# Kernel optimization log

Hardware: AMD Instinct MI355X
Metric: run time of the kernel (lower is better)

The kernel has to match this reference:

```python
import jax, jax.numpy as jnp
import numpy as np

PH = PW = 16  # patch size


def setup_inputs() -> dict:
    key = jax.random.key(0)
    k1, k2, k3, k4, k5 = jax.random.split(key, 5)
    B, N, D, V = 8, 4096, 768, 10240
    x = jax.random.uniform(k1, (B, N, D), dtype=jnp.float32)          # (B, N, ph*pw*C) in [0,1)
    patch_coord = jax.random.randint(k2, (B, N, 2), 0, 64).astype(jnp.int64)  # (y, x) grid coords
    patch_valid = jax.random.randint(k3, (B, N), 0, 2).astype(bool)
    proj_w = jax.random.normal(k4, (D, D), dtype=jnp.float32) * 0.02  # Linear weight (out, in), no bias
    pos_table = jax.random.normal(k5, (2, V, D), dtype=jnp.float32) * 0.02
    return {"x": x, "patch_coord": patch_coord, "patch_valid": patch_valid,
            "proj_w": proj_w, "pos_table": pos_table}


def reference(x, patch_coord, patch_valid, proj_w, pos_table):
    B, N, PPC = x.shape
    C = PPC // (PH * PW)
    # Reorder patch pixels from (ph, pw, C) flat order to (C, ph, pw) flat order.
    x = x.reshape(B, N, PH, PW, C).transpose(0, 1, 4, 2, 3).reshape(B, N, PPC)
    x = 2.0 * (x - 0.5)
    x = jnp.einsum('bnk,dk->bnd', x, proj_w)  # Linear, bias=False
    # External (y, x) -> internal (x, y)
    position_ids = patch_coord[..., ::-1]
    clamped = jnp.maximum(position_ids, 0)
    # Equivalent to one_hot(clamped) @ table summed over the 2 coord axes.
    pos = pos_table[0][clamped[..., 0]] + pos_table[1][clamped[..., 1]]  # (B, N, D)
    padding_positions = ~patch_valid
    pos = jnp.where(padding_positions[..., None], 0.0, pos)
    return x + pos, position_ids, padding_positions
```

## Files before the change

### kernel.cpp

```cpp
#include <hip/hip_runtime.h>
#include <hip/hip_bf16.h>
#include <cstddef>

#define D_DIM 768
#define V_DIM 10240
#define ROWS 32768
#define BM 128
#define BN 128
#define BK 32

using bf16x8 = __attribute__((ext_vector_type(8))) __bf16;
using f32x4  = __attribute__((ext_vector_type(4))) float;

__global__ void prep_w(const float* __restrict__ W, __bf16* __restrict__ Wp,
                       float* __restrict__ bias) {
    __shared__ float row[D_DIM];
    __shared__ float red[256];
    const int d = blockIdx.x;
    const int t = threadIdx.x;
    float s = 0.f;
    for (int k = t; k < D_DIM; k += 256) {
        float w = W[(size_t)d * D_DIM + k];
        row[k] = w;
        s += w;
    }
    red[t] = s;
    __syncthreads();
    for (int off = 128; off > 0; off >>= 1) {
        if (t < off) red[t] += red[t + off];
        __syncthreads();
    }
    if (t == 0) bias[d] = -red[0];
    for (int j = t; j < D_DIM; j += 256) {
        int c  = j % 3;
        int pw = (j / 3) & 15;
        int ph = j / 48;
        Wp[(size_t)d * D_DIM + j] = (__bf16)(2.0f * row[c * 256 + ph * 16 + pw]);
    }
}

__global__ void conv_aux(const float* __restrict__ X, __bf16* __restrict__ Xb,
                         const int* __restrict__ coord, const int* __restrict__ valid,
                         float* __restrict__ out1, float* __restrict__ out2) {
    int i = blockIdx.x * blockDim.x + threadIdx.x;
    size_t base = (size_t)i * 8;
    const float4* src = (const float4*)(X + base);
    float4 f0 = src[0];
    float4 f1 = src[1];
    bf16x8 v;
    v[0] = (__bf16)f0.x; v[1] = (__bf16)f0.y; v[2] = (__bf16)f0.z; v[3] = (__bf16)f0.w;
    v[4] = (__bf16)f1.x; v[5] = (__bf16)f1.y; v[6] = (__bf16)f1.z; v[7] = (__bf16)f1.w;
    *(bf16x8*)(Xb + base) = v;

    if (i < ROWS) {
        int c0 = coord[2 * i];
        int c1 = coord[2 * i + 1];
        out1[2 * i]     = (float)c1;
        out1[2 * i + 1] = (float)c0;
        out2[i] = valid[i] ? 0.0f : 1.0f;
    }
}

__global__ void aux_out(const int* __restrict__ coord, const int* __restrict__ valid,
                        float* __restrict__ out1, float* __restrict__ out2) {
    int i = blockIdx.x * blockDim.x + threadIdx.x;
    if (i < ROWS) {
        int c0 = coord[2 * i];
        int c1 = coord[2 * i + 1];
        out1[2 * i]     = (float)c1;
        out1[2 * i + 1] = (float)c0;
        out2[i] = valid[i] ? 0.0f : 1.0f;
    }
}

__launch_bounds__(256)
__global__ void gemm_fast(const __bf16* __restrict__ Xb, const __bf16* __restrict__ Wp,
                          const float* __restrict__ bias, const float* __restrict__ ptab,
                          const int* __restrict__ coord, const int* __restrict__ valid,
                          float* __restrict__ out) {
    __shared__ __align__(16) __bf16 la[BM * BK];
    __shared__ __align__(16) __bf16 lb[BN * BK];

    const int id  = blockIdx.x;
    const int xcd = id & 7;
    const int j6  = id >> 3;
    const int p   = xcd * 32 + j6 / 6;
    const int c   = j6 % 6;
    const int m0  = p * BM;
    const int n0  = c * BN;

    const int tid  = threadIdx.x;
    const int lane = tid & 63;
    const int wave = tid >> 6;
    const int wr   = (wave >> 1) * 64;
    const int wc   = (wave & 1) * 64;
    const int lr   = lane & 15;
    const int qh   = lane >> 4;

    const __bf16* srcA[2];
    const __bf16* srcB[2];
    int dst[2];
    #pragma unroll
    for (int i = 0; i < 2; ++i) {
        int q   = i * 256 + tid;
        int row = q >> 2;
        int un  = (q & 3) ^ ((row >> 1) & 3);
        srcA[i] = Xb + (size_t)(m0 + row) * D_DIM + un * 8;
        srcB[i] = Wp + (size_t)(n0 + row) * D_DIM + un * 8;
        dst[i]  = q * 8;
    }

    int aoff[4], boff[4];
    #pragma unroll
    for (int i = 0; i < 4; ++i) {
        int rowa = wr + i * 16 + lr;
        aoff[i] = rowa * BK + ((qh ^ ((rowa >> 1) & 3)) * 8);
        int rowb = wc + i * 16 + lr;
        boff[i] = rowb * BK + ((qh ^ ((rowb >> 1) & 3)) * 8);
    }

    f32x4 acc[4][4] = {};

    for (int kt = 0; kt < D_DIM / BK; ++kt) {
        const int k0 = kt * BK;

        #pragma unroll
        for (int i = 0; i < 2; ++i) {
            __builtin_amdgcn_global_load_lds(
                (const __attribute__((address_space(1))) void*)(srcA[i] + k0),
                (__attribute__((address_space(3))) void*)&la[dst[i]], 16, 0, 0);
            __builtin_amdgcn_global_load_lds(
                (const __attribute__((address_space(1))) void*)(srcB[i] + k0),
                (__attribute__((address_space(3))) void*)&lb[dst[i]], 16, 0, 0);
        }

        __syncthreads();

        bf16x8 af[4], bfr[4];
        #pragma unroll
        for (int i = 0; i < 4; ++i)
            af[i] = *(const bf16x8*)&la[aoff[i]];
        #pragma unroll
        for (int j = 0; j < 4; ++j)
            bfr[j] = *(const bf16x8*)&lb[boff[j]];

        #pragma unroll
        for (int i = 0; i < 4; ++i)
            #pragma unroll
            for (int j = 0; j < 4; ++j)
                acc[i][j] = __builtin_amdgcn_mfma_f32_16x16x32_bf16(af[i], bfr[j], acc[i][j], 0, 0, 0);

        __syncthreads();
    }

    const float* pt0 = ptab;
    const float* pt1 = ptab + (size_t)V_DIM * D_DIM;
    const int rq = (lane >> 4) * 4;

    float bvals[4];
    #pragma unroll
    for (int j = 0; j < 4; ++j)
        bvals[j] = bias[n0 + wc + j * 16 + lr];

    #pragma unroll
    for (int i = 0; i < 4; ++i) {
        #pragma unroll
        for (int r = 0; r < 4; ++r) {
            int m = m0 + wr + i * 16 + rq + r;
            int c0 = coord[2 * m];
            int c1 = coord[2 * m + 1];
            if (c0 < 0) c0 = 0;
            if (c1 < 0) c1 = 0;
            int vld = valid[m];
            #pragma unroll
            for (int j = 0; j < 4; ++j) {
                int d = n0 + wc + j * 16 + lr;
                float v = acc[i][j][r] + bvals[j];
                if (vld)
                    v += pt0[(size_t)c1 * D_DIM + d] + pt1[(size_t)c0 * D_DIM + d];
                out[(size_t)m * D_DIM + d] = v;
            }
        }
    }
}

__launch_bounds__(256)
__global__ void gemm_slow(const float* __restrict__ X, const __bf16* __restrict__ Wp,
                          const float* __restrict__ bias, const float* __restrict__ ptab,
                          const int* __restrict__ coord, const int* __restrict__ valid,
                          float* __restrict__ out) {
    __shared__ __align__(16) __bf16 la[BM * BK];
    __shared__ __align__(16) __bf16 lb[BN * BK];

    const int n0 = blockIdx.x * BN;
    const int m0 = blockIdx.y * BM;

    const int tid  = threadIdx.x;
    const int lane = tid & 63;
    const int wave = tid >> 6;
    const int wr   = (wave >> 1) * 64;
    const int wc   = (wave & 1) * 64;
    const int lr   = lane & 15;
    const int kq   = (lane >> 4) * 8;

    f32x4 acc[4][4] = {};

    for (int kt = 0; kt < D_DIM / BK; ++kt) {
        const int k0 = kt * BK;

        #pragma unroll
        for (int i = 0; i < 2; ++i) {
            int idx = i * 2048 + tid * 8;
            int row = idx >> 5;
            int col = idx & 31;
            const __bf16* src = Wp + (size_t)(n0 + row) * D_DIM + k0 + col;
            __builtin_amdgcn_global_load_lds(
                (const __attribute__((address_space(1))) void*)src,
                (__attribute__((address_space(3))) void*)&lb[idx], 16, 0, 0);
        }

        #pragma unroll
        for (int i = 0; i < 2; ++i) {
            int idx = i * 2048 + tid * 8;
            int row = idx >> 5;
            int col = idx & 31;
            const float4* src = (const float4*)(X + (size_t)(m0 + row) * D_DIM + k0 + col);
            float4 f0 = src[0];
            float4 f1 = src[1];
            bf16x8 v;
            v[0] = (__bf16)f0.x; v[1] = (__bf16)f0.y; v[2] = (__bf16)f0.z; v[3] = (__bf16)f0.w;
            v[4] = (__bf16)f1.x; v[5] = (__bf16)f1.y; v[6] = (__bf16)f1.z; v[7] = (__bf16)f1.w;
            *(bf16x8*)&la[idx] = v;
        }

        __syncthreads();

        bf16x8 af[4], bfr[4];
        #pragma unroll
        for (int i = 0; i < 4; ++i)
            af[i] = *(const bf16x8*)&la[(wr + i * 16 + lr) * BK + kq];
        #pragma unroll
        for (int j = 0; j < 4; ++j)
            bfr[j] = *(const bf16x8*)&lb[(wc + j * 16 + lr) * BK + kq];

        #pragma unroll
        for (int i = 0; i < 4; ++i)
            #pragma unroll
            for (int j = 0; j < 4; ++j)
                acc[i][j] = __builtin_amdgcn_mfma_f32_16x16x32_bf16(af[i], bfr[j], acc[i][j], 0, 0, 0);

        __syncthreads();
    }

    const float* pt0 = ptab;
    const float* pt1 = ptab + (size_t)V_DIM * D_DIM;
    const int rq = (lane >> 4) * 4;

    float bvals[4];
    #pragma unroll
    for (int j = 0; j < 4; ++j)
        bvals[j] = bias[n0 + wc + j * 16 + lr];

    #pragma unroll
    for (int i = 0; i < 4; ++i) {
        #pragma unroll
        for (int r = 0; r < 4; ++r) {
            int m = m0 + wr + i * 16 + rq + r;
            int c0 = coord[2 * m];
            int c1 = coord[2 * m + 1];
            if (c0 < 0) c0 = 0;
            if (c1 < 0) c1 = 0;
            int vld = valid[m];
            #pragma unroll
            for (int j = 0; j < 4; ++j) {
                int d = n0 + wc + j * 16 + lr;
                float v = acc[i][j][r] + bvals[j];
                if (vld)
                    v += pt0[(size_t)c1 * D_DIM + d] + pt1[(size_t)c0 * D_DIM + d];
                out[(size_t)m * D_DIM + d] = v;
            }
        }
    }
}

extern "C" void kernel_launch(void* const* d_in, const int* in_sizes, int n_in,
                              void* d_out, int out_size, void* d_ws, size_t ws_size,
                              hipStream_t stream) {
    const float* x     = (const float*)d_in[0];
    const int*   coord = (const int*)d_in[1];
    const int*   valid = (const int*)d_in[2];
    const float* W     = (const float*)d_in[3];
    const float* ptab  = (const float*)d_in[4];

    float* out0 = (float*)d_out;
    float* out1 = out0 + (size_t)ROWS * D_DIM;
    float* out2 = out1 + (size_t)ROWS * 2;

    const size_t xb_bytes = (size_t)ROWS * D_DIM * sizeof(__bf16);
    const size_t wp_bytes = (size_t)D_DIM * D_DIM * sizeof(__bf16);
    const size_t need = xb_bytes + wp_bytes + D_DIM * sizeof(float);

    if (ws_size >= need) {
        __bf16* Xb  = (__bf16*)d_ws;
        __bf16* Wp  = (__bf16*)((char*)d_ws + xb_bytes);
        float* bias = (float*)((char*)d_ws + xb_bytes + wp_bytes);

        hipLaunchKernelGGL(prep_w, dim3(D_DIM), dim3(256), 0, stream, W, Wp, bias);
        hipLaunchKernelGGL(conv_aux, dim3((ROWS * D_DIM / 8) / 256), dim3(256), 0, stream,
                           x, Xb, coord, valid, out1, out2);
        hipLaunchKernelGGL(gemm_fast, dim3((ROWS / BM) * (D_DIM / BN)), dim3(256), 0, stream,
                           Xb, Wp, bias, ptab, coord, valid, out0);
    } else {
        __bf16* Wp  = (__bf16*)d_ws;
        float* bias = (float*)((char*)d_ws + wp_bytes);

        hipLaunchKernelGGL(prep_w, dim3(D_DIM), dim3(256), 0, stream, W, Wp, bias);
        hipLaunchKernelGGL(aux_out, dim3(ROWS / 256), dim3(256), 0, stream, coord, valid, out1, out2);
        hipLaunchKernelGGL(gemm_slow, dim3(D_DIM / BN, ROWS / BM), dim3(256), 0, stream,
                           x, Wp, bias, ptab, coord, valid, out0);
    }
}
```

Measured before the change: 274.3 us.

## Triple-buffer LDS tiles in bf16 GEMM with async global-to-LDS prefetch

The single-buffered K loop, which waited on every tile load before computing, becomes a three-stage LDS ring. Loads for tile k+2 are issued while tile k is computed, with vmcnt waits and one barrier per step in place of two syncthreads. This is meant to hide global-load latency behind MFMA work. It triples LDS use (48KB per block), which may lower occupancy, and it relies on hand-counted vmcnt values staying correct.

```diff
diff --git a/kernel.cpp b/kernel.cpp
--- a/kernel.cpp
+++ b/kernel.cpp
@@ -8,6 +8,8 @@
 #define BM 128
 #define BN 128
 #define BK 32
+#define KTILES (D_DIM / BK)
+#define SZ (BM * BK)
 
 using bf16x8 = __attribute__((ext_vector_type(8))) __bf16;
 using f32x4  = __attribute__((ext_vector_type(4))) float;
@@ -78,8 +80,8 @@
                           const float* __restrict__ bias, const float* __restrict__ ptab,
                           const int* __restrict__ coord, const int* __restrict__ valid,
                           float* __restrict__ out) {
-    __shared__ __align__(16) __bf16 la[BM * BK];
-    __shared__ __align__(16) __bf16 lb[BN * BK];
+    __shared__ __align__(16) __bf16 la[3 * SZ];
+    __shared__ __align__(16) __bf16 lb[3 * SZ];
 
     const int id  = blockIdx.x;
     const int xcd = id & 7;
@@ -121,37 +123,60 @@
 
     f32x4 acc[4][4] = {};
 
-    for (int kt = 0; kt < D_DIM / BK; ++kt) {
-        const int k0 = kt * BK;
-
-        #pragma unroll
-        for (int i = 0; i < 2; ++i) {
-            __builtin_amdgcn_global_load_lds(
-                (const __attribute__((address_space(1))) void*)(srcA[i] + k0),
-                (__attribute__((address_space(3))) void*)&la[dst[i]], 16, 0, 0);
-            __builtin_amdgcn_global_load_lds(
-                (const __attribute__((address_space(1))) void*)(srcB[i] + k0),
-                (__attribute__((address_space(3))) void*)&lb[dst[i]], 16, 0, 0);
-        }
-
-        __syncthreads();
-
-        bf16x8 af[4], bfr[4];
-        #pragma unroll
-        for (int i = 0; i < 4; ++i)
-            af[i] = *(const bf16x8*)&la[aoff[i]];
-        #pragma unroll
-        for (int j = 0; j < 4; ++j)
-            bfr[j] = *(const bf16x8*)&lb[boff[j]];
-
-        #pragma unroll
-        for (int i = 0; i < 4; ++i)
-            #pragma unroll
-            for (int j = 0; j < 4; ++j)
-                acc[i][j] = __builtin_amdgcn_mfma_f32_16x16x32_bf16(af[i], bfr[j], acc[i][j], 0, 0, 0);
-
-        __syncthreads();
-    }
+#define STAGE(OFF, KT)                                                          \
+    do {                                                                        \
+        const int k0_ = (KT) * BK;                                              \
+        _Pragma("unroll")                                                       \
+        for (int i_ = 0; i_ < 2; ++i_) {                                        \
+            __builtin_amdgcn_global_load_lds(                                   \
+                (const __attribute__((address_space(1))) void*)(srcA[i_] + k0_),\
+                (__attribute__((address_space(3))) void*)&la[(OFF) + dst[i_]],  \
+                16, 0, 0);                                                      \
+            __builtin_amdgcn_global_load_lds(                                   \
+                (const __attribute__((address_space(1))) void*)(srcB[i_] + k0_),\
+                (__attribute__((address_space(3))) void*)&lb[(OFF) + dst[i_]],  \
+                16, 0, 0);                                                      \
+        }                                                                       \
+    } while (0)
+
+#define COMPUTE(OFF)                                                            \
+    do {                                                                        \
+        bf16x8 af_[4], bf_[4];                                                  \
+        _Pragma("unroll")                                                       \
+        for (int i_ = 0; i_ < 4; ++i_) {                                        \
+            af_[i_] = *(const bf16x8*)&la[(OFF) + aoff[i_]];                    \
+            bf_[i_] = *(const bf16x8*)&lb[(OFF) + boff[i_]];                    \
+        }                                                                       \
+        _Pragma("unroll")                                                       \
+        for (int i_ = 0; i_ < 4; ++i_)                                          \
+            _Pragma("unroll")                                                   \
+            for (int j_ = 0; j_ < 4; ++j_)                                      \
+                acc[i_][j_] = __builtin_amdgcn_mfma_f32_16x16x32_bf16(          \
+                    af_[i_], bf_[j_], acc[i_][j_], 0, 0, 0);                    \
+    } while (0)
+
+#define VMCNT4 asm volatile("s_waitcnt vmcnt(4)" ::: "memory")
+#define VMCNT0 asm volatile("s_waitcnt vmcnt(0)" ::: "memory")
+#define BAR    __builtin_amdgcn_s_barrier()
+
+    STAGE(0, 0);
+    STAGE(SZ, 1);
+
+    for (int t = 0; t < 7; ++t) {
+        const int kb = 3 * t;
+        VMCNT4; BAR; STAGE(2 * SZ, kb + 2); COMPUTE(0);
+        VMCNT4; BAR; STAGE(0,      kb + 3); COMPUTE(SZ);
+        VMCNT4; BAR; STAGE(SZ,     kb + 4); COMPUTE(2 * SZ);
+    }
+    VMCNT4; BAR; STAGE(2 * SZ, 23); COMPUTE(0);
+    VMCNT4; BAR; COMPUTE(SZ);
+    VMCNT0; BAR; COMPUTE(2 * SZ);
+
+#undef STAGE
+#undef COMPUTE
+#undef VMCNT4
+#undef VMCNT0
+#undef BAR
 
     const float* pt0 = ptab;
     const float* pt1 = ptab + (size_t)V_DIM * D_DIM;
```

Result: slower. 291.1 us (+6.1%).
